# Kernel optimization log

Hardware: AMD Instinct MI355X
Metric: run time of the kernel (lower is better)

## Reference

```python
import jax, jax.numpy as jnp
import numpy as np

N = 1_000_000      # occupied input voxels
NREF = 400_000     # occupied reference (target) voxels on the stride-2 grid
CIN = 32
COUT = 64
G = 256            # input spatial grid extent per axis
B = 4              # batch size (ME batch index in coords[:, 0])
PRIME = 2654435761 # odd -> bijective multiplier mod 2^26


def _decode_np(ids, g):
    z = ids % g; ids = ids // g
    y = ids % g; ids = ids // g
    x = ids % g; b = ids // g
    return np.stack([b, x, y, z], axis=1).astype(np.int32)


def setup_inputs() -> dict:
    key = jax.random.key(0)
    k1, k2, k3 = jax.random.split(key, 3)
    # unique input voxel coordinates on a B x G^3 grid (bijection mod 2^26)
    ids_in = (np.arange(N, dtype=np.int64) * PRIME) % (B * G ** 3)
    coords = _decode_np(ids_in, G)                      # [N,4] (b,x,y,z), unique
    # unique reference coordinates on the stride-2 output grid
    gh = G // 2
    ids_ref = (np.arange(NREF, dtype=np.int64) * PRIME) % (B * gh ** 3)
    ref = _decode_np(ids_ref, gh)
    ref[:, 1:] *= 2                                     # ME tensor-stride-2 coords
    feats = jax.random.normal(k1, (N, CIN), jnp.float32)
    W = jax.random.normal(k2, (8, CIN, COUT), jnp.float32) * (1.0 / np.sqrt(8 * CIN))
    b = jax.random.normal(k3, (COUT,), jnp.float32) * 0.01
    return {"feats": feats, "W": W, "b": b,
            "coords": jnp.asarray(coords), "ref_coords": jnp.asarray(ref)}


def _ravel(c, step):
    # faithful to get_target_by_sp_tensor: batch-major ravel of 4 columns
    return c[:, 3] + c[:, 2] * step + c[:, 1] * step * step + c[:, 0] * step * step * step


def reference(feats, W, b, coords, ref_coords):
    n = coords.shape[0]
    # --- hash table of input voxels (sorted keys + permuted features) ---
    in_key = ((coords[:, 0] * G + coords[:, 1]) * G + coords[:, 2]) * G + coords[:, 3]
    order = jnp.argsort(in_key)
    skeys = in_key[order]
    sfeats = feats[order]
    # --- output coordinates: stride-2 downsample (kernel=2, stride=2) ---
    p = coords.at[:, 1:].set((coords[:, 1:] // 2) * 2)
    pkey = ((p[:, 0] * G + p[:, 1]) * G + p[:, 2]) * G + p[:, 3]
    out_key = jnp.unique(pkey, size=n, fill_value=-1)   # sorted, padded with -1
    valid = out_key >= 0
    ok = jnp.where(valid, out_key, 0)
    oz = ok % G; r = ok // G
    oy = r % G; r = r // G
    ox = r % G; ob = r // G
    out_coords = jnp.where(valid[:, None], jnp.stack([ob, ox, oy, oz], axis=1), -1)
    # --- sparse conv: gather the 2x2x2 children of each output voxel ---
    acc = jnp.zeros((n, W.shape[2]), feats.dtype)
    offsets = [(dx, dy, dz) for dx in (0, 1) for dy in (0, 1) for dz in (0, 1)]
    for i, (dx, dy, dz) in enumerate(offsets):
        ckey = out_key + dx * G * G + dy * G + dz
        idx = jnp.clip(jnp.searchsorted(skeys, ckey), 0, n - 1)
        found = (skeys[idx] == ckey) & valid
        f = jnp.where(found[:, None], sfeats[idx], 0.0)
        acc = acc + f @ W[i]
    out_feats = jnp.where(valid[:, None], acc + b, 0.0)
    # --- pruning mask: ravel + isin, faithful to get_target_by_sp_tensor ---
    step = jnp.maximum(out_coords.max(), ref_coords.max()).astype(jnp.int32) + 1
    min_value = jnp.minimum(out_coords.min(), ref_coords.min())
    shift = jnp.where(min_value < 0, -min_value, 0)
    oc = out_coords.at[:, 1:].add(shift)
    rc = ref_coords.at[:, 1:].add(shift)
    out1d = _ravel(oc, step)
    ref1d = _ravel(rc, step)
    sref = jnp.sort(ref1d)
    j = jnp.clip(jnp.searchsorted(sref, out1d), 0, sref.shape[0] - 1)
    mask = (sref[j] == out1d) & valid
    out_feats = jnp.where(mask[:, None], out_feats, 0.0)
    return out_coords, out_feats, mask
```

## Files before the change

kernel.cpp:

```cpp
#include <hip/hip_runtime.h>

#define WORDS_P  (1u << 18)
#define NBLK2    1024

__device__ __forceinline__ unsigned k23_of(int b, int x, int y, int z) {
  return ((unsigned)b << 21) | ((unsigned)(x >> 1) << 14) |
         ((unsigned)(y >> 1) << 7) | (unsigned)(z >> 1);
}

__global__ __launch_bounds__(256) void fill_all(float4* __restrict__ wsz, size_t n4_ws,
                                                float4* __restrict__ ofm, size_t n4_ofm,
                                                float4* __restrict__ oc, size_t n4_oc) {
  size_t stride = (size_t)gridDim.x * 256u;
  size_t i0 = (size_t)blockIdx.x * 256u + threadIdx.x;
  float4 z = make_float4(0.f, 0.f, 0.f, 0.f);
  float4 m1 = make_float4(-1.f, -1.f, -1.f, -1.f);
  for (size_t i = i0; i < n4_ws; i += stride) wsz[i] = z;
  for (size_t i = i0; i < n4_ofm; i += stride) ofm[i] = z;
  for (size_t i = i0; i < n4_oc; i += stride) oc[i] = m1;
}

__global__ __launch_bounds__(256) void build_bm(const int4* __restrict__ coords, int n,
                                                const int4* __restrict__ ref, int nref,
                                                unsigned* __restrict__ parbm,
                                                unsigned* __restrict__ refbm, int nbN) {
  if ((int)blockIdx.x < nbN) {
    int i = blockIdx.x * 256 + threadIdx.x;
    if (i >= n) return;
    int4 c = coords[i];
    unsigned k = k23_of(c.x, c.y, c.z, c.w);
    atomicOr(&parbm[k >> 5], 1u << (k & 31));
  } else {
    int i = (blockIdx.x - nbN) * 256 + threadIdx.x;
    if (i >= nref) return;
    int4 c = ref[i];
    unsigned k = k23_of(c.x, c.y, c.z, c.w);
    atomicOr(&refbm[k >> 5], 1u << (k & 31));
  }
}

__global__ __launch_bounds__(256) void pop2(const unsigned* __restrict__ parbm,
                                            unsigned* __restrict__ refbm,
                                            unsigned* __restrict__ bsums) {
  __shared__ unsigned s[256];
  unsigned t = threadIdx.x;
  unsigned w = blockIdx.x * 256u + t;
  unsigned p = parbm[w];
  unsigned m = p & refbm[w];
  refbm[w] = m;
  s[t] = __popc(p); __syncthreads();
  for (int off = 128; off > 0; off >>= 1) { if (t < (unsigned)off) s[t] += s[t + off]; __syncthreads(); }
  if (t == 0) bsums[blockIdx.x] = s[0];
  __syncthreads();
  s[t] = __popc(m); __syncthreads();
  for (int off = 128; off > 0; off >>= 1) { if (t < (unsigned)off) s[t] += s[t + off]; __syncthreads(); }
  if (t == 0) bsums[NBLK2 + blockIdx.x] = s[0];
}

__global__ __launch_bounds__(256) void scan2(const unsigned* __restrict__ bsums,
                                             unsigned* __restrict__ bscan,
                                             unsigned* __restrict__ counter) {
  __shared__ unsigned s[256];
  unsigned a = blockIdx.x;
  const unsigned* src = bsums + a * NBLK2;
  unsigned* dst = bscan + a * NBLK2;
  unsigned t = threadIdx.x;
  unsigned loc[4], sum = 0;
#pragma unroll
  for (int k = 0; k < 4; k++) { loc[k] = src[t * 4 + k]; sum += loc[k]; }
  s[t] = sum; __syncthreads();
  for (int off = 1; off < 256; off <<= 1) {
    unsigned v = (t >= (unsigned)off) ? s[t - off] : 0u;
    __syncthreads(); s[t] += v; __syncthreads();
  }
  if (a == 1u && t == 255u) counter[0] = s[255];
  unsigned excl = (t == 0) ? 0u : s[t - 1];
#pragma unroll
  for (int k = 0; k < 4; k++) { dst[t * 4 + k] = excl; excl += loc[k]; }
}

__global__ __launch_bounds__(256) void prefix2(const unsigned* __restrict__ parbm,
                                               const unsigned* __restrict__ maskbm,
                                               const unsigned* __restrict__ bscan,
                                               unsigned* __restrict__ parpre,
                                               unsigned* __restrict__ maskpre) {
  __shared__ unsigned s[256];
  unsigned t = threadIdx.x;
  unsigned w = blockIdx.x * 256u + t;
  unsigned cp = __popc(parbm[w]);
  s[t] = cp; __syncthreads();
  for (int off = 1; off < 256; off <<= 1) {
    unsigned v = (t >= (unsigned)off) ? s[t - off] : 0u;
    __syncthreads(); s[t] += v; __syncthreads();
  }
  parpre[w] = ((t == 0) ? 0u : s[t - 1]) + bscan[blockIdx.x];
  __syncthreads();
  unsigned cm = __popc(maskbm[w]);
  s[t] = cm; __syncthreads();
  for (int off = 1; off < 256; off <<= 1) {
    unsigned v = (t >= (unsigned)off) ? s[t - off] : 0u;
    __syncthreads(); s[t] += v; __syncthreads();
  }
  maskpre[w] = ((t == 0) ? 0u : s[t - 1]) + bscan[NBLK2 + blockIdx.x];
}

__global__ __launch_bounds__(256) void scatter_emit(const int4* __restrict__ coords, int n,
                                                    const unsigned* __restrict__ parbm,
                                                    const unsigned* __restrict__ parpre,
                                                    const unsigned* __restrict__ maskbm,
                                                    const unsigned* __restrict__ maskpre,
                                                    unsigned* __restrict__ clist,
                                                    unsigned* __restrict__ mrow,
                                                    float4* __restrict__ out_coords,
                                                    float* __restrict__ out_mask,
                                                    int nbN) {
  if ((int)blockIdx.x < nbN) {
    int i = blockIdx.x * 256 + threadIdx.x;
    if (i >= n) return;
    int4 c = coords[i];
    unsigned k = k23_of(c.x, c.y, c.z, c.w);
    unsigned w = k >> 5, b = k & 31u;
    unsigned mw = maskbm[w];
    if ((mw >> b) & 1u) {
      unsigned j = maskpre[w] + __popc(mw & ((1u << b) - 1u));
      unsigned off = (((unsigned)c.y & 1u) << 2) | (((unsigned)c.z & 1u) << 1) |
                     ((unsigned)c.w & 1u);
      clist[j * 8u + off] = (unsigned)i + 1u;
    }
    return;
  }
  unsigned w = (blockIdx.x - nbN) * 256u + threadIdx.x;
  unsigned bits = parbm[w];
  if (!bits) return;
  unsigned mb = maskbm[w];
  unsigned r = parpre[w];
  unsigned j = maskpre[w];
  while (bits) {
    unsigned b = (unsigned)__ffs((int)bits) - 1u;
    bits &= bits - 1u;
    unsigned k = (w << 5) | b;
    float bb = (float)(k >> 21);
    float x = (float)(((k >> 14) & 127u) << 1);
    float y = (float)(((k >> 7) & 127u) << 1);
    float z = (float)((k & 127u) << 1);
    out_coords[r] = make_float4(bb, x, y, z);
    if ((mb >> b) & 1u) {
      out_mask[r] = 1.0f;
      mrow[j++] = r;
    }
    r++;
  }
}

__global__ __launch_bounds__(1024, 8) void conv_lds(const float* __restrict__ feats,
                                                    const float* __restrict__ Wg,
                                                    const float* __restrict__ bias,
                                                    const unsigned* __restrict__ clist,
                                                    const unsigned* __restrict__ mrow,
                                                    const unsigned* __restrict__ counter,
                                                    float* __restrict__ out_feats) {
  __shared__ float lw[16384];
  for (unsigned t = threadIdx.x; t < 4096u; t += 1024u)
    ((float4*)lw)[t] = ((const float4*)Wg)[t];
  __syncthreads();

  unsigned lane = threadIdx.x & 63u;
  unsigned wave = blockIdx.x * 16u + (threadIdx.x >> 6);
  unsigned nwaves = gridDim.x * 16u;
  unsigned M = counter[0];
  float bv = bias[lane];
  for (unsigned j = wave; j < M; j += nwaves) {
    unsigned r = mrow[j];
    uint4 c0 = *(const uint4*)(clist + (size_t)j * 8u);
    uint4 c1 = *(const uint4*)(clist + (size_t)j * 8u + 4u);
    unsigned cs[8] = {c0.x, c0.y, c0.z, c0.w, c1.x, c1.y, c1.z, c1.w};
    float acc = bv;
#pragma unroll
    for (int i = 0; i < 8; i++) {
      unsigned v = (unsigned)__builtin_amdgcn_readfirstlane((int)cs[i]);
      if (v) {
        const float* f = feats + (size_t)(v - 1u) * 32u;
        const float* wl = lw + i * 2048 + lane;
#pragma unroll
        for (int k = 0; k < 32; k++) acc = fmaf(f[k], wl[k * 64], acc);
      }
    }
    out_feats[(size_t)r * 64u + lane] = acc;
  }
}

extern "C" void kernel_launch(void* const* d_in, const int* in_sizes, int n_in,
                              void* d_out, int out_size, void* d_ws, size_t ws_size,
                              hipStream_t stream) {
  const float* feats = (const float*)d_in[0];
  const float* W     = (const float*)d_in[1];
  const float* bias  = (const float*)d_in[2];
  const int4*  coords = (const int4*)d_in[3];
  const int4*  ref    = (const int4*)d_in[4];
  int N    = in_sizes[0] / 32;
  int NREF = in_sizes[4] / 4;

  float* out_coords = (float*)d_out;
  float* out_feats  = out_coords + (size_t)N * 4;
  float* out_mask   = out_feats + (size_t)N * 64;

  char* ws = (char*)d_ws;
  unsigned* parbm   = (unsigned*)(ws);
  unsigned* refbm   = (unsigned*)(ws + (1u << 20));
  unsigned* maskbm  = refbm;
  unsigned* clist   = (unsigned*)(ws + (2u << 20));
  unsigned* parpre  = (unsigned*)(ws + (15u << 20));
  unsigned* maskpre = (unsigned*)(ws + (16u << 20));
  unsigned* mrow    = (unsigned*)(ws + (17u << 20));
  unsigned* bsums   = (unsigned*)(ws + (19u << 20));
  unsigned* bscan   = (unsigned*)(ws + (19u << 20) + 16384);
  unsigned* counter = (unsigned*)(ws + (19u << 20) + 32768);

  int nbN = (N + 255) / 256;
  int nbR = (NREF + 255) / 256;

  fill_all<<<2048, 256, 0, stream>>>((float4*)ws, (size_t)(15u << 20) / 16u,
                                     (float4*)out_feats, (size_t)N * 65u * 4u / 16u,
                                     (float4*)out_coords, (size_t)N);
  build_bm<<<nbN + nbR, 256, 0, stream>>>(coords, N, ref, NREF, parbm, refbm, nbN);
  pop2<<<NBLK2, 256, 0, stream>>>(parbm, refbm, bsums);
  scan2<<<2, 256, 0, stream>>>(bsums, bscan, counter);
  prefix2<<<NBLK2, 256, 0, stream>>>(parbm, maskbm, bscan, parpre, maskpre);
  scatter_emit<<<nbN + NBLK2, 256, 0, stream>>>(coords, N, parbm, parpre, maskbm,
                                                maskpre, clist, mrow,
                                                (float4*)out_coords, out_mask, nbN);
  conv_lds<<<512, 1024, 0, stream>>>(feats, W, bias, clist, mrow, counter, out_feats);
}
```

Before: 149.8 us.

## Shrink workspace zero-fill, fuse block scan into prefix, fill only coord tail

The blanket zero-fill of the 15 MB workspace is cut to just the 2 MB of bitmaps. The clist entries are now zeroed only for used rows inside the prefix kernel, which also absorbs the separate two-block scan by having each block sum the preceding block totals. The -1 fill of output coordinates moves into extra scatter_emit blocks that write only the tail past the number of occupied parents. Output feature zeroing uses nontemporal stores. This removes one launch and a large share of memory writes, in exchange for redundant bsums reads per block and per-thread serial clist zeroing loops.

Result: no change. 150.6 us (+0.5%).

```diff
diff --git a/kernel.cpp b/kernel.cpp
--- a/kernel.cpp
+++ b/kernel.cpp
@@ -2,22 +2,24 @@
 
 #define WORDS_P  (1u << 18)
 #define NBLK2    1024
+
+typedef float f4_native __attribute__((ext_vector_type(4)));
 
 __device__ __forceinline__ unsigned k23_of(int b, int x, int y, int z) {
   return ((unsigned)b << 21) | ((unsigned)(x >> 1) << 14) |
          ((unsigned)(y >> 1) << 7) | (unsigned)(z >> 1);
 }
 
-__global__ __launch_bounds__(256) void fill_all(float4* __restrict__ wsz, size_t n4_ws,
-                                                float4* __restrict__ ofm, size_t n4_ofm,
-                                                float4* __restrict__ oc, size_t n4_oc) {
+__global__ __launch_bounds__(256) void fill_all(f4_native* __restrict__ wsz, size_t n4_ws,
+                                                f4_native* __restrict__ ofm, size_t n4_ofm) {
   size_t stride = (size_t)gridDim.x * 256u;
   size_t i0 = (size_t)blockIdx.x * 256u + threadIdx.x;
-  float4 z = make_float4(0.f, 0.f, 0.f, 0.f);
-  float4 m1 = make_float4(-1.f, -1.f, -1.f, -1.f);
-  for (size_t i = i0; i < n4_ws; i += stride) wsz[i] = z;
-  for (size_t i = i0; i < n4_ofm; i += stride) ofm[i] = z;
-  for (size_t i = i0; i < n4_oc; i += stride) oc[i] = m1;
+  f4_native z = {0.f, 0.f, 0.f, 0.f};
+  size_t total = n4_ws + n4_ofm;
+  for (size_t i = i0; i < total; i += stride) {
+    if (i < n4_ws) wsz[i] = z;
+    else __builtin_nontemporal_store(z, &ofm[i - n4_ws]);
+  }
 }
 
 __global__ __launch_bounds__(256) void build_bm(const int4* __restrict__ coords, int n,
@@ -57,51 +59,55 @@
   if (t == 0) bsums[NBLK2 + blockIdx.x] = s[0];
 }
 
-__global__ __launch_bounds__(256) void scan2(const unsigned* __restrict__ bsums,
-                                             unsigned* __restrict__ bscan,
-                                             unsigned* __restrict__ counter) {
+__global__ __launch_bounds__(256) void prefix2b(const unsigned* __restrict__ parbm,
+                                                const unsigned* __restrict__ maskbm,
+                                                const unsigned* __restrict__ bsums,
+                                                unsigned* __restrict__ parpre,
+                                                unsigned* __restrict__ maskpre,
+                                                unsigned* __restrict__ clist,
+                                                unsigned* __restrict__ counter) {
   __shared__ unsigned s[256];
-  unsigned a = blockIdx.x;
-  const unsigned* src = bsums + a * NBLK2;
-  unsigned* dst = bscan + a * NBLK2;
-  unsigned t = threadIdx.x;
-  unsigned loc[4], sum = 0;
-#pragma unroll
-  for (int k = 0; k < 4; k++) { loc[k] = src[t * 4 + k]; sum += loc[k]; }
-  s[t] = sum; __syncthreads();
-  for (int off = 1; off < 256; off <<= 1) {
-    unsigned v = (t >= (unsigned)off) ? s[t - off] : 0u;
-    __syncthreads(); s[t] += v; __syncthreads();
-  }
-  if (a == 1u && t == 255u) counter[0] = s[255];
-  unsigned excl = (t == 0) ? 0u : s[t - 1];
-#pragma unroll
-  for (int k = 0; k < 4; k++) { dst[t * 4 + k] = excl; excl += loc[k]; }
-}
-
-__global__ __launch_bounds__(256) void prefix2(const unsigned* __restrict__ parbm,
-                                               const unsigned* __restrict__ maskbm,
-                                               const unsigned* __restrict__ bscan,
-                                               unsigned* __restrict__ parpre,
-                                               unsigned* __restrict__ maskpre) {
-  __shared__ unsigned s[256];
-  unsigned t = threadIdx.x;
-  unsigned w = blockIdx.x * 256u + t;
-  unsigned cp = __popc(parbm[w]);
+  __shared__ unsigned basP_s, basM_s;
+  unsigned t = threadIdx.x, blk = blockIdx.x;
+  unsigned accP = 0, accM = 0;
+  for (unsigned idx = t; idx < blk; idx += 256u) {
+    accP += bsums[idx];
+    accM += bsums[NBLK2 + idx];
+  }
+  s[t] = accP; __syncthreads();
+  for (int off = 128; off > 0; off >>= 1) { if (t < (unsigned)off) s[t] += s[t + off]; __syncthreads(); }
+  if (t == 0) basP_s = s[0];
+  __syncthreads();
+  s[t] = accM; __syncthreads();
+  for (int off = 128; off > 0; off >>= 1) { if (t < (unsigned)off) s[t] += s[t + off]; __syncthreads(); }
+  if (t == 0) basM_s = s[0];
+  __syncthreads();
+  unsigned basP = basP_s, basM = basM_s;
+
+  unsigned w = blk * 256u + t;
+  unsigned pw = parbm[w], mw = maskbm[w];
+  unsigned cp = __popc(pw), cm = __popc(mw);
   s[t] = cp; __syncthreads();
   for (int off = 1; off < 256; off <<= 1) {
     unsigned v = (t >= (unsigned)off) ? s[t - off] : 0u;
     __syncthreads(); s[t] += v; __syncthreads();
   }
-  parpre[w] = ((t == 0) ? 0u : s[t - 1]) + bscan[blockIdx.x];
-  __syncthreads();
-  unsigned cm = __popc(maskbm[w]);
+  unsigned ppre = basP + ((t == 0) ? 0u : s[t - 1]);
+  parpre[w] = ppre;
+  unsigned plast = basP + s[255];
+  __syncthreads();
   s[t] = cm; __syncthreads();
   for (int off = 1; off < 256; off <<= 1) {
     unsigned v = (t >= (unsigned)off) ? s[t - off] : 0u;
     __syncthreads(); s[t] += v; __syncthreads();
   }
-  maskpre[w] = ((t == 0) ? 0u : s[t - 1]) + bscan[NBLK2 + blockIdx.x];
+  unsigned mpre = basM + ((t == 0) ? 0u : s[t - 1]);
+  maskpre[w] = mpre;
+  for (unsigned k = 0; k < cm * 8u; k++) clist[mpre * 8u + k] = 0u;
+  if (blk == NBLK2 - 1u && t == 255u) {
+    counter[0] = basM + s[255];
+    counter[1] = plast;
+  }
 }
 
 __global__ __launch_bounds__(256) void scatter_emit(const int4* __restrict__ coords, int n,
@@ -109,6 +115,7 @@
                                                     const unsigned* __restrict__ parpre,
                                                     const unsigned* __restrict__ maskbm,
                                                     const unsigned* __restrict__ maskpre,
+                                                    const unsigned* __restrict__ counter,
                                                     unsigned* __restrict__ clist,
                                                     unsigned* __restrict__ mrow,
                                                     float4* __restrict__ out_coords,
@@ -129,27 +136,35 @@
     }
     return;
   }
-  unsigned w = (blockIdx.x - nbN) * 256u + threadIdx.x;
-  unsigned bits = parbm[w];
-  if (!bits) return;
-  unsigned mb = maskbm[w];
-  unsigned r = parpre[w];
-  unsigned j = maskpre[w];
-  while (bits) {
-    unsigned b = (unsigned)__ffs((int)bits) - 1u;
-    bits &= bits - 1u;
-    unsigned k = (w << 5) | b;
-    float bb = (float)(k >> 21);
-    float x = (float)(((k >> 14) & 127u) << 1);
-    float y = (float)(((k >> 7) & 127u) << 1);
-    float z = (float)((k & 127u) << 1);
-    out_coords[r] = make_float4(bb, x, y, z);
-    if ((mb >> b) & 1u) {
-      out_mask[r] = 1.0f;
-      mrow[j++] = r;
+  if ((int)blockIdx.x < nbN + (int)NBLK2) {
+    unsigned w = (blockIdx.x - nbN) * 256u + threadIdx.x;
+    unsigned bits = parbm[w];
+    if (!bits) return;
+    unsigned mb = maskbm[w];
+    unsigned r = parpre[w];
+    unsigned j = maskpre[w];
+    while (bits) {
+      unsigned b = (unsigned)__ffs((int)bits) - 1u;
+      bits &= bits - 1u;
+      unsigned k = (w << 5) | b;
+      float bb = (float)(k >> 21);
+      float x = (float)(((k >> 14) & 127u) << 1);
+      float y = (float)(((k >> 7) & 127u) << 1);
+      float z = (float)((k & 127u) << 1);
+      out_coords[r] = make_float4(bb, x, y, z);
+      if ((mb >> b) & 1u) {
+        out_mask[r] = 1.0f;
+        mrow[j++] = r;
+      }
+      r++;
     }
-    r++;
-  }
+    return;
+  }
+  unsigned P = counter[1];
+  unsigned idx = (blockIdx.x - nbN - NBLK2) * 256u + threadIdx.x;
+  unsigned ntail = (unsigned)n - P;
+  float4 m1 = make_float4(-1.f, -1.f, -1.f, -1.f);
+  for (unsigned i = idx; i < ntail; i += 64u * 256u) out_coords[P + i] = m1;
 }
 
 __global__ __launch_bounds__(1024, 8) void conv_lds(const float* __restrict__ feats,
@@ -213,21 +228,19 @@
   unsigned* maskpre = (unsigned*)(ws + (16u << 20));
   unsigned* mrow    = (unsigned*)(ws + (17u << 20));
   unsigned* bsums   = (unsigned*)(ws + (19u << 20));
-  unsigned* bscan   = (unsigned*)(ws + (19u << 20) + 16384);
-  unsigned* counter = (unsigned*)(ws + (19u << 20) + 32768);
+  unsigned* counter = (unsigned*)(ws + (19u << 20) + 16384);
 
   int nbN = (N + 255) / 256;
   int nbR = (NREF + 255) / 256;
 
-  fill_all<<<2048, 256, 0, stream>>>((float4*)ws, (size_t)(15u << 20) / 16u,
-                                     (float4*)out_feats, (size_t)N * 65u * 4u / 16u,
-                                     (float4*)out_coords, (size_t)N);
+  fill_all<<<2048, 256, 0, stream>>>((f4_native*)ws, (size_t)(2u << 20) / 16u,
+                                     (f4_native*)out_feats, (size_t)N * 65u * 4u / 16u);
   build_bm<<<nbN + nbR, 256, 0, stream>>>(coords, N, ref, NREF, parbm, refbm, nbN);
   pop2<<<NBLK2, 256, 0, stream>>>(parbm, refbm, bsums);
-  scan2<<<2, 256, 0, stream>>>(bsums, bscan, counter);
-  prefix2<<<NBLK2, 256, 0, stream>>>(parbm, maskbm, bscan, parpre, maskpre);
-  scatter_emit<<<nbN + NBLK2, 256, 0, stream>>>(coords, N, parbm, parpre, maskbm,
-                                                maskpre, clist, mrow,
-                                                (float4*)out_coords, out_mask, nbN);
+  prefix2b<<<NBLK2, 256, 0, stream>>>(parbm, maskbm, bsums, parpre, maskpre, clist,
+                                      counter);
+  scatter_emit<<<nbN + NBLK2 + 64, 256, 0, stream>>>(coords, N, parbm, parpre, maskbm,
+                                                     maskpre, counter, clist, mrow,
+                                                     (float4*)out_coords, out_mask, nbN);
   conv_lds<<<512, 1024, 0, stream>>>(feats, W, bias, clist, mrow, counter, out_feats);
 }
```
